# Kernel optimization log

Measured on AMD Instinct MI355X. Metric: run time of the kernel, lower is better.

Reference implementation:

```python
import jax, jax.numpy as jnp
import numpy as np

NUM_RELATION = 7

def setup_inputs() -> dict:
    key = jax.random.key(0)
    ks = jax.random.split(key, 12)
    N, E, D, DO, R, DE = 20000, 640000, 512, 512, NUM_RELATION, 59
    inp = {
        "node_feat": jax.random.normal(ks[0], (N, D), dtype=jnp.float32),
        "edge_weight": jax.random.uniform(ks[1], (E,), dtype=jnp.float32),
        "edge_feat": jax.random.normal(ks[2], (E, DE), dtype=jnp.float32),
        "W_lin": jax.random.normal(ks[3], (DO, R * D), dtype=jnp.float32) * 0.02,
        "b_lin": jax.random.normal(ks[4], (DO,), dtype=jnp.float32) * 0.02,
        "W_self": jax.random.normal(ks[5], (DO, D), dtype=jnp.float32) * 0.02,
        "b_self": jax.random.normal(ks[6], (DO,), dtype=jnp.float32) * 0.02,
        "W_edge": jax.random.normal(ks[7], (DO, DE), dtype=jnp.float32) * 0.02,
        "b_edge": jax.random.normal(ks[8], (DO,), dtype=jnp.float32) * 0.02,
        "node_in": jax.random.randint(ks[9], (E,), 0, N, dtype=jnp.int64) if jax.config.jax_enable_x64 else jax.random.randint(ks[9], (E,), 0, N).astype(jnp.int32),
        "node_out": jax.random.randint(ks[10], (E,), 0, N).astype(jnp.int32),
        "relation": jax.random.randint(ks[11], (E,), 0, R).astype(jnp.int32),
    }
    inp["node_in"] = inp["node_in"].astype(jnp.int32)
    return inp


def reference(node_feat, edge_weight, edge_feat, W_lin, b_lin, W_self, b_self,
              W_edge, b_edge, node_in, node_out, relation):
    N, D = node_feat.shape
    R = NUM_RELATION
    # segment id: node_out * R + relation  (column index in sparse (N, N*R) adjacency)
    seg = node_out * R + relation  # [E]
    # update = adjacency.T @ input  == scatter-add of weighted source features
    msg = node_feat[node_in] * edge_weight[:, None]               # [E, D]
    update = jax.ops.segment_sum(msg, seg, num_segments=N * R)    # [N*R, D]
    # edge_linear path: edge_update scattered with the same segment ids
    edge_msg = (edge_feat @ W_edge.T + b_edge) * edge_weight[:, None]  # [E, D]
    update = update + jax.ops.segment_sum(edge_msg, seg, num_segments=N * R)
    update = update.reshape(N, R * D)                             # [N, R*D]
    # combine: linear(update) + self_loop(input), then relu
    out = update @ W_lin.T + b_lin + node_feat @ W_self.T + b_self
    return jax.nn.relu(out)
```

## Files before the change

### kernel.cpp

```cpp
#include <hip/hip_runtime.h>
#include <stdint.h>

typedef unsigned short u16;
typedef __attribute__((ext_vector_type(8))) __bf16 bf16x8;
typedef __attribute__((ext_vector_type(4))) float f32x4;

#define NREL 7
#define DIM  512
#define DEDGE 59
#define KC   420
#define KCP  448
#define KTOT 4544

__device__ __forceinline__ float bf2f(u16 u) {
  union { unsigned u; float f; } c; c.u = ((unsigned)u) << 16; return c.f;
}
__device__ __forceinline__ u16 f2bf(float f) {
  union { float f; unsigned u; } c; c.f = f;
  unsigned r = ((c.u >> 16) & 1u) + 0x7FFFu;
  return (u16)((c.u + r) >> 16);
}

__device__ __forceinline__ void gload16(const void* g, void* l) {
  __builtin_amdgcn_global_load_lds(
      (__attribute__((address_space(1))) void*)g,
      (__attribute__((address_space(3))) void*)l, 16, 0, 0);
}

__global__ void convA(const float* __restrict__ in, u16* __restrict__ out, int total4) {
  int i = blockIdx.x * 256 + threadIdx.x;
  if (i >= total4) return;
  float4 v = ((const float4*)in)[i];
  ushort4 r;
  r.x = f2bf(v.x); r.y = f2bf(v.y); r.z = f2bf(v.z); r.w = f2bf(v.w);
  ((ushort4*)out)[i] = r;
}

__global__ void buildBW(const float* __restrict__ W_lin, const float* __restrict__ W_self,
                        u16* __restrict__ Bfull, int total4) {
  int gid = blockIdx.x * 256 + threadIdx.x;
  if (gid >= total4) return;
  int idx = gid * 4;
  int o = idx >> 12;
  int k = idx & 4095;
  const float* src = (k < NREL * DIM) ? (W_lin + (size_t)o * (NREL * DIM) + k)
                                      : (W_self + (size_t)o * DIM + (k - NREL * DIM));
  float4 v = *(const float4*)src;
  ushort4 rr;
  rr.x = f2bf(v.x); rr.y = f2bf(v.y); rr.z = f2bf(v.z); rr.w = f2bf(v.w);
  *(ushort4*)(Bfull + (size_t)o * KTOT + k) = rr;
}

__global__ __launch_bounds__(512) void buildCx(const float* __restrict__ W_edge,
                                               const float* __restrict__ b_edge,
                                               const float* __restrict__ W_lin,
                                               u16* __restrict__ Bfull) {
  int c = blockIdx.x;
  int o = threadIdx.x;
  u16* dst = Bfull + (size_t)o * KTOT + NREL * DIM + DIM;
  if (c >= KC) { dst[c] = 0; return; }
  __shared__ float col[DIM];
  int r;
  if (c < NREL * DEDGE) {
    r = c / DEDGE;
    int de = c - r * DEDGE;
    col[o] = W_edge[(size_t)o * DEDGE + de];
  } else {
    r = c - NREL * DEDGE;
    col[o] = b_edge[o];
  }
  __syncthreads();
  const float* wrow = W_lin + (size_t)o * (NREL * DIM) + (size_t)r * DIM;
  float acc = 0.f;
#pragma unroll 8
  for (int d = 0; d < DIM; ++d) acc += col[d] * wrow[d];
  dst[c] = f2bf(acc);
}

__global__ void countK2(const int* __restrict__ node_out, const int* __restrict__ relation,
                        int* __restrict__ counts2, int E) {
  int e = blockIdx.x * 256 + threadIdx.x;
  if (e < E) atomicAdd(&counts2[node_out[e] * 8 + relation[e]], 1);
}

__global__ void scanNode(const int* __restrict__ counts2, int* __restrict__ counts, int N) {
  int n = blockIdx.x * 256 + threadIdx.x;
  if (n >= N) return;
  int s = 0;
#pragma unroll
  for (int r = 0; r < NREL; ++r) s += counts2[n * 8 + r];
  counts[n] = s;
}

__global__ __launch_bounds__(1024) void scanK(const int* __restrict__ counts,
                                              int* __restrict__ offs, int n) {
  __shared__ int lds[1024];
  int tid = threadIdx.x;
  int carry = 0;
  for (int base = 0; base < n; base += 1024) {
    int i = base + tid;
    int v = (i < n) ? counts[i] : 0;
    lds[tid] = v;
    __syncthreads();
    for (int o = 1; o < 1024; o <<= 1) {
      int t = (tid >= o) ? lds[tid - o] : 0;
      __syncthreads();
      lds[tid] += t;
      __syncthreads();
    }
    int excl = lds[tid] - v;
    if (i < n) offs[i] = carry + excl;
    int total = lds[1023];
    carry += total;
    __syncthreads();
  }
  if (tid == 0) offs[n] = carry;
}

__global__ void offs2K(const int* __restrict__ offs, const int* __restrict__ counts2,
                       int* __restrict__ offs2, int* __restrict__ cursor2, int N) {
  int n = blockIdx.x * 256 + threadIdx.x;
  if (n >= N) return;
  int base = offs[n];
#pragma unroll
  for (int r = 0; r < NREL; ++r) {
    offs2[n * 8 + r] = base;
    cursor2[n * 8 + r] = base;
    base += counts2[n * 8 + r];
  }
  offs2[n * 8 + 7] = base;
}

__global__ void fillK2(const int* __restrict__ node_in, const int* __restrict__ node_out,
                       const int* __restrict__ relation, const float* __restrict__ ew,
                       int* __restrict__ cursor2, int* __restrict__ eids,
                       uint2* __restrict__ pairs, int E) {
  int e = blockIdx.x * 256 + threadIdx.x;
  if (e >= E) return;
  int p = atomicAdd(&cursor2[node_out[e] * 8 + relation[e]], 1);
  eids[p] = e;
  pairs[p] = make_uint2((unsigned)node_in[e], __float_as_uint(ew[e]));
}

__global__ __launch_bounds__(64) void gatherG2(const float* __restrict__ ef,
                                               const int* __restrict__ eids,
                                               const uint2* __restrict__ pairs,
                                               const int* __restrict__ offs2,
                                               u16* __restrict__ Mfull) {
  int n = blockIdx.x;
  int lane = threadIdx.x;
  u16* row = Mfull + (size_t)n * KTOT + NREL * DIM + DIM;
  int base = n * 8;
  for (int r = 0; r < NREL; ++r) {
    int p0 = offs2[base + r], p1 = offs2[base + r + 1];
    float acc = 0.f;
    for (int p = p0; p < p1; ++p) {
      int e = __builtin_amdgcn_readfirstlane(eids[p]);
      float w = __uint_as_float(__builtin_amdgcn_readfirstlane(pairs[p].y));
      float v = (lane < DEDGE) ? ef[(size_t)e * DEDGE + lane] : 1.0f;
      acc += w * v;
    }
    if (lane < DEDGE) row[r * DEDGE + lane] = f2bf(acc);
    else if (lane == DEDGE) row[NREL * DEDGE + r] = f2bf(acc);
  }
  if (lane >= 60) {
    for (int c = KC + (lane - 60); c < KCP; c += 4) row[c] = 0;
  }
}

__global__ __launch_bounds__(128) void aggK(const u16* __restrict__ NF,
                                            const uint2* __restrict__ pairs,
                                            const int* __restrict__ offs2,
                                            u16* __restrict__ Mfull) {
  int n = blockIdx.x;
  int o0 = threadIdx.x * 4;
  u16* mrow = Mfull + (size_t)n * KTOT;
  *(ushort4*)(mrow + NREL * DIM + o0) = *(const ushort4*)(NF + (size_t)n * DIM + o0);
  int base = n * 8;
  for (int r = 0; r < NREL; ++r) {
    int p0 = offs2[base + r], p1 = offs2[base + r + 1];
    float a0 = 0.f, a1 = 0.f, a2 = 0.f, a3 = 0.f;
    for (int p = p0; p < p1; ++p) {
      uint2 pr = pairs[p];
      int src = __builtin_amdgcn_readfirstlane((int)pr.x);
      float w = __uint_as_float(__builtin_amdgcn_readfirstlane(pr.y));
      ushort4 hv = *(const ushort4*)(NF + (size_t)src * DIM + o0);
      a0 += w * bf2f(hv.x);
      a1 += w * bf2f(hv.y);
      a2 += w * bf2f(hv.z);
      a3 += w * bf2f(hv.w);
    }
    ushort4 st;
    st.x = f2bf(a0); st.y = f2bf(a1); st.z = f2bf(a2); st.w = f2bf(a3);
    *(ushort4*)(mrow + r * DIM + o0) = st;
  }
}

__global__ __launch_bounds__(256) void gemm_br(const u16* __restrict__ A,
                                               const u16* __restrict__ Bt,
                                               const float* __restrict__ b_lin,
                                               const float* __restrict__ b_self,
                                               float* __restrict__ Cout, int M) {
  __shared__ __align__(16) u16 sA[3][128 * 32];
  __shared__ __align__(16) u16 sB[3][128 * 32];
  const int tid = threadIdx.x;
  const int w = tid >> 6, l = tid & 63;
  const int lr = l & 15, kg = l >> 4;
  const int sl = kg ^ ((lr >> 1) & 3);

  const int id = blockIdx.x;
  const int npan = gridDim.x >> 2;
  const int nfull = (npan >> 3) << 3;
  int p, c;
  if (id < nfull * 4) {
    int g = id >> 5, r = id & 31;
    p = g * 8 + (r & 7);
    c = r >> 3;
  } else {
    int t = id - nfull * 4;
    p = nfull + (t >> 2);
    c = t & 3;
  }
  const int m0 = p * 128, n0 = c * 128;
  const int wr = w >> 1, wc = w & 1;
  f32x4 acc[4][4];
  const f32x4 z4 = {0.f, 0.f, 0.f, 0.f};
#pragma unroll
  for (int i = 0; i < 4; ++i)
#pragma unroll
    for (int j = 0; j < 4; ++j) acc[i][j] = z4;

  const int ktiles = KTOT / 32;

  auto stage = [&](int kt, int b) {
    const int k0 = kt * 32;
#pragma unroll
    for (int t = 0; t < 2; ++t) {
      int idx = w * 128 + t * 64 + l;
      int row = idx >> 2, kp = idx & 3;
      int s = kp ^ ((row >> 1) & 3);
      int gm = m0 + row; gm = gm < M ? gm : M - 1;
      gload16(A + (size_t)gm * KTOT + k0 + s * 8,
              (char*)sA[b] + (size_t)idx * 16);
    }
#pragma unroll
    for (int t = 0; t < 2; ++t) {
      int idx = w * 128 + t * 64 + l;
      int row = idx >> 2, kp = idx & 3;
      int s = kp ^ ((row >> 1) & 3);
      gload16(Bt + (size_t)(n0 + row) * KTOT + k0 + s * 8,
              (char*)sB[b] + (size_t)idx * 16);
    }
  };

  stage(0, 0);
  stage(1, 1);
  asm volatile("s_waitcnt vmcnt(4)" ::: "memory");
  __builtin_amdgcn_s_barrier();
  __builtin_amdgcn_sched_barrier(0);

  for (int kt = 0; kt < ktiles; ++kt) {
    const int cur = kt % 3;
    if (kt + 2 < ktiles) stage(kt + 2, (kt + 2) % 3);
    bf16x8 af[4], bfr[4];
#pragma unroll
    for (int i = 0; i < 4; ++i)
      af[i] = *(const bf16x8*)(sA[cur] + (size_t)(wr * 64 + i * 16 + lr) * 32 + sl * 8);
#pragma unroll
    for (int j = 0; j < 4; ++j)
      bfr[j] = *(const bf16x8*)(sB[cur] + (size_t)(wc * 64 + j * 16 + lr) * 32 + sl * 8);
#pragma unroll
    for (int i = 0; i < 4; ++i)
#pragma unroll
      for (int j = 0; j < 4; ++j)
        acc[i][j] = __builtin_amdgcn_mfma_f32_16x16x32_bf16(af[i], bfr[j], acc[i][j], 0, 0, 0);
    if (kt + 2 < ktiles) {
      asm volatile("s_waitcnt vmcnt(4)" ::: "memory");
    } else {
      asm volatile("s_waitcnt vmcnt(0)" ::: "memory");
    }
    __builtin_amdgcn_s_barrier();
    __builtin_amdgcn_sched_barrier(0);
  }
#pragma unroll
  for (int i = 0; i < 4; ++i) {
#pragma unroll
    for (int j = 0; j < 4; ++j) {
      int gj = n0 + wc * 64 + j * 16 + lr;
      float bias = b_lin[gj] + b_self[gj];
#pragma unroll
      for (int v = 0; v < 4; ++v) {
        int gm = m0 + wr * 64 + i * 16 + kg * 4 + v;
        if (gm < M)
          ((float*)Cout)[(size_t)gm * DIM + gj] = fmaxf(acc[i][j][v] + bias, 0.f);
      }
    }
  }
}

extern "C" void kernel_launch(void* const* d_in, const int* in_sizes, int n_in,
                              void* d_out, int out_size, void* d_ws, size_t ws_size,
                              hipStream_t stream) {
  const float* node_feat = (const float*)d_in[0];
  const float* edge_weight = (const float*)d_in[1];
  const float* edge_feat = (const float*)d_in[2];
  const float* W_lin = (const float*)d_in[3];
  const float* b_lin = (const float*)d_in[4];
  const float* W_self = (const float*)d_in[5];
  const float* b_self = (const float*)d_in[6];
  const float* W_edge = (const float*)d_in[7];
  const float* b_edge = (const float*)d_in[8];
  const int* node_in = (const int*)d_in[9];
  const int* node_out = (const int*)d_in[10];
  const int* relation = (const int*)d_in[11];
  float* out = (float*)d_out;

  const int N = in_sizes[0] / DIM;
  const int E = in_sizes[1];

  char* ws = (char*)d_ws;
  size_t off = 0;
  auto take = [&](size_t b) {
    char* p = ws + off;
    off += (b + 255) & ~(size_t)255;
    return p;
  };
  u16* NF      = (u16*)take((size_t)N * DIM * 2);
  u16* Bfull   = (u16*)take((size_t)DIM * KTOT * 2);
  u16* Mfull   = (u16*)take((size_t)N * KTOT * 2);
  int* counts2 = (int*)take((size_t)N * 8 * 4);
  int* counts  = (int*)take((size_t)N * 4);
  int* offs    = (int*)take((size_t)(N + 1) * 4);
  int* offs2   = (int*)take((size_t)N * 8 * 4);
  int* cursor2 = (int*)take((size_t)N * 8 * 4);
  int* eids    = (int*)take((size_t)E * 4);
  uint2* pairs = (uint2*)take((size_t)E * 8);
  if (off > ws_size) return;

  hipMemsetAsync(counts2, 0, (size_t)N * 8 * 4, stream);

  {
    int total4 = N * DIM / 4;
    convA<<<(total4 + 255) / 256, 256, 0, stream>>>(node_feat, NF, total4);
  }
  {
    int total4 = DIM * 4096 / 4;
    buildBW<<<(total4 + 255) / 256, 256, 0, stream>>>(W_lin, W_self, Bfull, total4);
  }
  buildCx<<<KCP, 512, 0, stream>>>(W_edge, b_edge, W_lin, Bfull);

  countK2<<<(E + 255) / 256, 256, 0, stream>>>(node_out, relation, counts2, E);
  scanNode<<<(N + 255) / 256, 256, 0, stream>>>(counts2, counts, N);
  scanK<<<1, 1024, 0, stream>>>(counts, offs, N);
  offs2K<<<(N + 255) / 256, 256, 0, stream>>>(offs, counts2, offs2, cursor2, N);
  fillK2<<<(E + 255) / 256, 256, 0, stream>>>(node_in, node_out, relation, edge_weight,
                                              cursor2, eids, pairs, E);

  gatherG2<<<N, 64, 0, stream>>>(edge_feat, eids, pairs, offs2, Mfull);
  aggK<<<N, 128, 0, stream>>>(NF, pairs, offs2, Mfull);

  {
    int npan = (N + 127) / 128;
    gemm_br<<<npan * 4, 256, 0, stream>>>(Mfull, Bfull, b_lin, b_self, out, N);
  }
}
```

Baseline: 516.9 us.

## Replace prefix scan with atomic base allocation, pack edge records, widen aggregation

```diff
diff --git a/kernel.cpp b/kernel.cpp
--- a/kernel.cpp
+++ b/kernel.cpp
@@ -3,6 +3,7 @@
 
 typedef unsigned short u16;
 typedef __attribute__((ext_vector_type(8))) __bf16 bf16x8;
+typedef __attribute__((ext_vector_type(8))) unsigned short u16x8;
 typedef __attribute__((ext_vector_type(4))) float f32x4;
 
 #define NREL 7
@@ -83,68 +84,35 @@
   if (e < E) atomicAdd(&counts2[node_out[e] * 8 + relation[e]], 1);
 }
 
-__global__ void scanNode(const int* __restrict__ counts2, int* __restrict__ counts, int N) {
+__global__ void baseK(const int* __restrict__ counts2, int* __restrict__ offs2,
+                      int* __restrict__ cursor2, int* __restrict__ totalCtr, int N) {
   int n = blockIdx.x * 256 + threadIdx.x;
   if (n >= N) return;
+  int cnt[NREL];
   int s = 0;
 #pragma unroll
-  for (int r = 0; r < NREL; ++r) s += counts2[n * 8 + r];
-  counts[n] = s;
-}
-
-__global__ __launch_bounds__(1024) void scanK(const int* __restrict__ counts,
-                                              int* __restrict__ offs, int n) {
-  __shared__ int lds[1024];
-  int tid = threadIdx.x;
-  int carry = 0;
-  for (int base = 0; base < n; base += 1024) {
-    int i = base + tid;
-    int v = (i < n) ? counts[i] : 0;
-    lds[tid] = v;
-    __syncthreads();
-    for (int o = 1; o < 1024; o <<= 1) {
-      int t = (tid >= o) ? lds[tid - o] : 0;
-      __syncthreads();
-      lds[tid] += t;
-      __syncthreads();
-    }
-    int excl = lds[tid] - v;
-    if (i < n) offs[i] = carry + excl;
-    int total = lds[1023];
-    carry += total;
-    __syncthreads();
-  }
-  if (tid == 0) offs[n] = carry;
-}
-
-__global__ void offs2K(const int* __restrict__ offs, const int* __restrict__ counts2,
-                       int* __restrict__ offs2, int* __restrict__ cursor2, int N) {
-  int n = blockIdx.x * 256 + threadIdx.x;
-  if (n >= N) return;
-  int base = offs[n];
+  for (int r = 0; r < NREL; ++r) { cnt[r] = counts2[n * 8 + r]; s += cnt[r]; }
+  int base = atomicAdd(totalCtr, s);
 #pragma unroll
   for (int r = 0; r < NREL; ++r) {
     offs2[n * 8 + r] = base;
     cursor2[n * 8 + r] = base;
-    base += counts2[n * 8 + r];
+    base += cnt[r];
   }
   offs2[n * 8 + 7] = base;
 }
 
 __global__ void fillK2(const int* __restrict__ node_in, const int* __restrict__ node_out,
                        const int* __restrict__ relation, const float* __restrict__ ew,
-                       int* __restrict__ cursor2, int* __restrict__ eids,
-                       uint2* __restrict__ pairs, int E) {
+                       int* __restrict__ cursor2, uint4* __restrict__ quads, int E) {
   int e = blockIdx.x * 256 + threadIdx.x;
   if (e >= E) return;
   int p = atomicAdd(&cursor2[node_out[e] * 8 + relation[e]], 1);
-  eids[p] = e;
-  pairs[p] = make_uint2((unsigned)node_in[e], __float_as_uint(ew[e]));
+  quads[p] = make_uint4((unsigned)node_in[e], __float_as_uint(ew[e]), (unsigned)e, 0u);
 }
 
 __global__ __launch_bounds__(64) void gatherG2(const float* __restrict__ ef,
-                                               const int* __restrict__ eids,
-                                               const uint2* __restrict__ pairs,
+                                               const uint4* __restrict__ quads,
                                                const int* __restrict__ offs2,
                                                u16* __restrict__ Mfull) {
   int n = blockIdx.x;
@@ -155,8 +123,9 @@
     int p0 = offs2[base + r], p1 = offs2[base + r + 1];
     float acc = 0.f;
     for (int p = p0; p < p1; ++p) {
-      int e = __builtin_amdgcn_readfirstlane(eids[p]);
-      float w = __uint_as_float(__builtin_amdgcn_readfirstlane(pairs[p].y));
+      uint4 q = quads[p];
+      int e = __builtin_amdgcn_readfirstlane((int)q.z);
+      float w = __uint_as_float(__builtin_amdgcn_readfirstlane(q.y));
       float v = (lane < DEDGE) ? ef[(size_t)e * DEDGE + lane] : 1.0f;
       acc += w * v;
     }
@@ -168,31 +137,35 @@
   }
 }
 
-__global__ __launch_bounds__(128) void aggK(const u16* __restrict__ NF,
-                                            const uint2* __restrict__ pairs,
+__global__ __launch_bounds__(256) void aggK(const u16* __restrict__ NF,
+                                            const uint4* __restrict__ quads,
                                             const int* __restrict__ offs2,
                                             u16* __restrict__ Mfull) {
   int n = blockIdx.x;
-  int o0 = threadIdx.x * 4;
+  int wid = threadIdx.x >> 6, lane = threadIdx.x & 63;
+  int o0 = lane * 8;
   u16* mrow = Mfull + (size_t)n * KTOT;
-  *(ushort4*)(mrow + NREL * DIM + o0) = *(const ushort4*)(NF + (size_t)n * DIM + o0);
+  if (wid == 3) {
+    *(u16x8*)(mrow + NREL * DIM + o0) = *(const u16x8*)(NF + (size_t)n * DIM + o0);
+  }
   int base = n * 8;
-  for (int r = 0; r < NREL; ++r) {
+  for (int r = wid; r < NREL; r += 4) {
     int p0 = offs2[base + r], p1 = offs2[base + r + 1];
-    float a0 = 0.f, a1 = 0.f, a2 = 0.f, a3 = 0.f;
+    float a[8];
+#pragma unroll
+    for (int j = 0; j < 8; ++j) a[j] = 0.f;
     for (int p = p0; p < p1; ++p) {
-      uint2 pr = pairs[p];
-      int src = __builtin_amdgcn_readfirstlane((int)pr.x);
-      float w = __uint_as_float(__builtin_amdgcn_readfirstlane(pr.y));
-      ushort4 hv = *(const ushort4*)(NF + (size_t)src * DIM + o0);
-      a0 += w * bf2f(hv.x);
-      a1 += w * bf2f(hv.y);
-      a2 += w * bf2f(hv.z);
-      a3 += w * bf2f(hv.w);
-    }
-    ushort4 st;
-    st.x = f2bf(a0); st.y = f2bf(a1); st.z = f2bf(a2); st.w = f2bf(a3);
-    *(ushort4*)(mrow + r * DIM + o0) = st;
+      uint4 q = quads[p];
+      int src = __builtin_amdgcn_readfirstlane((int)q.x);
+      float w = __uint_as_float(__builtin_amdgcn_readfirstlane(q.y));
+      u16x8 hv = *(const u16x8*)(NF + (size_t)src * DIM + o0);
+#pragma unroll
+      for (int j = 0; j < 8; ++j) a[j] += w * bf2f(hv[j]);
+    }
+    u16x8 st;
+#pragma unroll
+    for (int j = 0; j < 8; ++j) st[j] = f2bf(a[j]);
+    *(u16x8*)(mrow + r * DIM + o0) = st;
   }
 }
 
@@ -325,19 +298,18 @@
     off += (b + 255) & ~(size_t)255;
     return p;
   };
-  u16* NF      = (u16*)take((size_t)N * DIM * 2);
-  u16* Bfull   = (u16*)take((size_t)DIM * KTOT * 2);
-  u16* Mfull   = (u16*)take((size_t)N * KTOT * 2);
-  int* counts2 = (int*)take((size_t)N * 8 * 4);
-  int* counts  = (int*)take((size_t)N * 4);
-  int* offs    = (int*)take((size_t)(N + 1) * 4);
-  int* offs2   = (int*)take((size_t)N * 8 * 4);
-  int* cursor2 = (int*)take((size_t)N * 8 * 4);
-  int* eids    = (int*)take((size_t)E * 4);
-  uint2* pairs = (uint2*)take((size_t)E * 8);
+  u16* NF       = (u16*)take((size_t)N * DIM * 2);
+  u16* Bfull    = (u16*)take((size_t)DIM * KTOT * 2);
+  u16* Mfull    = (u16*)take((size_t)N * KTOT * 2);
+  int* counts2  = (int*)take((size_t)N * 8 * 4);
+  int* offs2    = (int*)take((size_t)N * 8 * 4);
+  int* cursor2  = (int*)take((size_t)N * 8 * 4);
+  int* totalCtr = (int*)take(256);
+  uint4* quads  = (uint4*)take((size_t)E * 16);
   if (off > ws_size) return;
 
   hipMemsetAsync(counts2, 0, (size_t)N * 8 * 4, stream);
+  hipMemsetAsync(totalCtr, 0, 256, stream);
 
   {
     int total4 = N * DIM / 4;
@@ -350,14 +322,12 @@
   buildCx<<<KCP, 512, 0, stream>>>(W_edge, b_edge, W_lin, Bfull);
 
   countK2<<<(E + 255) / 256, 256, 0, stream>>>(node_out, relation, counts2, E);
-  scanNode<<<(N + 255) / 256, 256, 0, stream>>>(counts2, counts, N);
-  scanK<<<1, 1024, 0, stream>>>(counts, offs, N);
-  offs2K<<<(N + 255) / 256, 256, 0, stream>>>(offs, counts2, offs2, cursor2, N);
+  baseK<<<(N + 255) / 256, 256, 0, stream>>>(counts2, offs2, cursor2, totalCtr, N);
   fillK2<<<(E + 255) / 256, 256, 0, stream>>>(node_in, node_out, relation, edge_weight,
-                                              cursor2, eids, pairs, E);
-
-  gatherG2<<<N, 64, 0, stream>>>(edge_feat, eids, pairs, offs2, Mfull);
-  aggK<<<N, 128, 0, stream>>>(NF, pairs, offs2, Mfull);
+                                              cursor2, quads, E);
+
+  gatherG2<<<N, 64, 0, stream>>>(edge_feat, quads, offs2, Mfull);
+  aggK<<<N, 256, 0, stream>>>(NF, quads, offs2, Mfull);
 
   {
     int npan = (N + 127) / 128;
```

Result: faster. 490.3 us (-5.2%).
